# Performance work log

Hardware: AMD Instinct MI355X
Metric: run time of the kernel (lower is better)

The kernel has to match this reference:

```python
import jax, jax.numpy as jnp
import numpy as np

D = 1024        # d_hidden
DE = 512        # d_expert (routed)
E = 8           # n_routed_experts
TOP_K = 2
DS = DE * 2     # shared expert width = d_expert * n_shared_experts


def setup_inputs() -> dict:
    key = jax.random.key(0)
    ks = jax.random.split(key, 8)
    s = 1.0 / np.sqrt(D)
    return {
        "x": jax.random.normal(ks[0], (2, 1024, D), dtype=jnp.float32),
        "W_g": jax.random.normal(ks[1], (D, E), dtype=jnp.float32) * s,
        "Wg_e": jax.random.normal(ks[2], (E, D, DE), dtype=jnp.float32) * s,
        "Wu_e": jax.random.normal(ks[3], (E, D, DE), dtype=jnp.float32) * s,
        "Wd_e": jax.random.normal(ks[4], (E, DE, D), dtype=jnp.float32) * (1.0 / np.sqrt(DE)),
        "Wg_s": jax.random.normal(ks[5], (D, DS), dtype=jnp.float32) * s,
        "Wu_s": jax.random.normal(ks[6], (D, DS), dtype=jnp.float32) * s,
        "Wd_s": jax.random.normal(ks[7], (DS, D), dtype=jnp.float32) * (1.0 / np.sqrt(DS)),
    }


def _moe(x, W_g, Wg_e, Wu_e, Wd_e, Wg_s, Wu_s, Wd_s):
    B, T, Dm = x.shape
    N = B * T
    xf = x.reshape(N, Dm)

    # shared expert (SwiGLU)
    shared = (jax.nn.silu(xf @ Wg_s) * (xf @ Wu_s)) @ Wd_s  # [N, D]

    # gating: softmax then top-k (set membership identical to torch sorted=False)
    probs = jax.nn.softmax(xf @ W_g, axis=-1)               # [N, E]
    topk_vals, topk_ids = jax.lax.top_k(probs, TOP_K)       # [N, K]

    # combine weights c[n, e] = sum of topk_vals where routed to expert e
    # (equivalent to the original gather -> weighted scatter_add combine)
    c = jnp.zeros((N, E), dtype=x.dtype)
    c = c.at[jnp.arange(N)[:, None], topk_ids].add(topk_vals)

    # dense per-expert SwiGLU, weighted-combined (same math as gather/scatter loop)
    gate = jax.nn.silu(jnp.einsum('nd,edh->neh', xf, Wg_e))
    up = jnp.einsum('nd,edh->neh', xf, Wu_e)
    routed = jnp.einsum('neh,ne,ehd->nd', gate * up, c, Wd_e)  # [N, D]

    return (shared + routed).reshape(B, T, Dm)


def reference(x, W_g, Wg_e, Wu_e, Wd_e, Wg_s, Wu_s, Wd_s):
    return _moe(x, W_g, Wg_e, Wu_e, Wd_e, Wg_s, Wu_s, Wd_s)
```

## Files before the change

### kernel.cpp

```cpp
#include <hip/hip_runtime.h>
#include <hip/hip_bf16.h>

#define NTOK 2048
#define DIM  1024
#define DEXP 512
#define NEXP 8
#define DSH  1024
#define KH   5120
#define MAXROWS 5120

typedef __hip_bfloat16 bf16;
typedef __attribute__((ext_vector_type(8))) short bf16x8;
typedef __attribute__((ext_vector_type(4))) float floatx4;

__device__ __forceinline__ void gl_lds16(const bf16* g, bf16* l) {
    __builtin_amdgcn_global_load_lds(
        (const __attribute__((address_space(1))) void*)g,
        (__attribute__((address_space(3))) void*)l, 16, 0, 0);
}

__device__ __forceinline__ float b2f(short s) {
    union { float f; unsigned u; } v;
    v.u = ((unsigned)(unsigned short)s) << 16;
    return v.f;
}

struct B4 { bf16 a, b, c, d; };

__global__ __launch_bounds__(256) void gate_logits(const float* __restrict__ x,
                                                   const float* __restrict__ Wg,
                                                   bf16* __restrict__ Xb,
                                                   int2* __restrict__ te,
                                                   float2* __restrict__ tp) {
    int t = blockIdx.x * 4 + (threadIdx.x >> 6);
    int lane = threadIdx.x & 63;
    const float* xr = x + (long)t * DIM;
    bf16* xo = Xb + (long)t * DIM;
    float acc[NEXP] = {0.f, 0.f, 0.f, 0.f, 0.f, 0.f, 0.f, 0.f};
#pragma unroll
    for (int i = 0; i < 4; i++) {
        int d = lane * 4 + i * 256;
        float4 xv = *(const float4*)(xr + d);
        B4 o{__float2bfloat16(xv.x), __float2bfloat16(xv.y),
             __float2bfloat16(xv.z), __float2bfloat16(xv.w)};
        *(B4*)(xo + d) = o;
#pragma unroll
        for (int j = 0; j < 4; j++) {
            float xs = (j == 0) ? xv.x : (j == 1) ? xv.y : (j == 2) ? xv.z : xv.w;
            float4 w0 = *(const float4*)(Wg + (d + j) * NEXP);
            float4 w1 = *(const float4*)(Wg + (d + j) * NEXP + 4);
            acc[0] += xs * w0.x; acc[1] += xs * w0.y; acc[2] += xs * w0.z; acc[3] += xs * w0.w;
            acc[4] += xs * w1.x; acc[5] += xs * w1.y; acc[6] += xs * w1.z; acc[7] += xs * w1.w;
        }
    }
#pragma unroll
    for (int e = 0; e < NEXP; e++)
#pragma unroll
        for (int off = 32; off; off >>= 1)
            acc[e] += __shfl_xor(acc[e], off);
    if (lane == 0) {
        float m = acc[0];
#pragma unroll
        for (int e = 1; e < NEXP; e++) m = fmaxf(m, acc[e]);
        float p[NEXP], s = 0.f;
#pragma unroll
        for (int e = 0; e < NEXP; e++) { p[e] = expf(acc[e] - m); s += p[e]; }
        float inv = 1.f / s;
#pragma unroll
        for (int e = 0; e < NEXP; e++) p[e] *= inv;
        int i1 = 0;
#pragma unroll
        for (int e = 1; e < NEXP; e++) if (p[e] > p[i1]) i1 = e;
        int i2 = (i1 == 0) ? 1 : 0;
#pragma unroll
        for (int e = 0; e < NEXP; e++) if (e != i1 && p[e] > p[i2]) i2 = e;
        te[t] = make_int2(i1, i2);
        tp[t] = make_float2(p[i1], p[i2]);
    }
}

__global__ __launch_bounds__(512) void assign_kernel(const int2* __restrict__ te,
                                                     const float2* __restrict__ tp,
                                                     int* __restrict__ counts,
                                                     int* __restrict__ offs,
                                                     int* __restrict__ tok_list,
                                                     float* __restrict__ cw,
                                                     int* __restrict__ s1a,
                                                     int* __restrict__ s2a) {
    __shared__ int cnt[NEXP];
    const int e = threadIdx.x >> 6;
    const int lane = threadIdx.x & 63;
    int base = 0;
    for (int t0 = 0; t0 < NTOK; t0 += 64) {
        int t = t0 + lane;
        int2 ee = te[t];
        bool m1 = (ee.x == e), m2 = (ee.y == e);
        bool mt = m1 || m2;
        unsigned long long mask = __ballot(mt);
        int pre = __popcll(mask & ((1ull << lane) - 1ull));
        if (mt) {
            int slot = base + pre;
            tok_list[e * NTOK + slot] = t;
            float2 pp = tp[t];
            cw[e * NTOK + slot] = m1 ? pp.x : pp.y;
            if (m1) s1a[t] = slot; else s2a[t] = slot;
        }
        base += __popcll(mask);
    }
    if (lane == 0) cnt[e] = base;
    __syncthreads();
    if (threadIdx.x == 0) {
        int o = 0;
#pragma unroll
        for (int i = 0; i < NEXP; i++) {
            counts[i] = cnt[i];
            offs[i] = o;
            o += (cnt[i] + 127) & ~127;
        }
    }
}

__global__ __launch_bounds__(256) void pack_weights(
        const float* __restrict__ Wg_s, const float* __restrict__ Wu_s,
        const float* __restrict__ Wg_e, const float* __restrict__ Wu_e,
        const float* __restrict__ Wd_s, const float* __restrict__ Wd_e,
        bf16* __restrict__ Bg, bf16* __restrict__ Bu, bf16* __restrict__ Bd) {
    __shared__ float t[32][36];
    int b = blockIdx.x;
    const float* src; bf16* dst; int C; long dstStride, dstBase; int tilesX;
    if (b < 1024)       { src = Wg_s; dst = Bg; C = 1024; dstStride = 1024; dstBase = 0; tilesX = 32; }
    else if (b < 2048)  { b -= 1024; src = Wu_s; dst = Bu; C = 1024; dstStride = 1024; dstBase = 0; tilesX = 32; }
    else if (b < 6144)  { b -= 2048; int z = b >> 9; b &= 511;
                          src = Wg_e + (long)z * DIM * DEXP; dst = Bg; C = 512;
                          dstStride = 1024; dstBase = (long)(DSH + z * DEXP) * 1024; tilesX = 16; }
    else if (b < 10240) { b -= 6144; int z = b >> 9; b &= 511;
                          src = Wu_e + (long)z * DIM * DEXP; dst = Bu; C = 512;
                          dstStride = 1024; dstBase = (long)(DSH + z * DEXP) * 1024; tilesX = 16; }
    else if (b < 11264) { b -= 10240; src = Wd_s; dst = Bd; C = 1024; dstStride = KH; dstBase = 0; tilesX = 32; }
    else                { b -= 11264; int z = b >> 9; b &= 511;
                          src = Wd_e + (long)z * DEXP * DIM; dst = Bd; C = 1024;
                          dstStride = KH; dstBase = DSH + (long)z * DEXP; tilesX = 32; }
    int tileX = b & (tilesX - 1), tileY = b / tilesX;
    int c0 = tileX * 32, r0 = tileY * 32;

    {
        int row = threadIdx.x >> 3, ch = threadIdx.x & 7;
        float4 v = *(const float4*)(src + (long)(r0 + row) * C + c0 + ch * 4);
        *(float4*)(&t[row][ch * 4]) = v;
    }
    __syncthreads();
    {
        int dc = threadIdx.x & 31, ch = threadIdx.x >> 5;
        int j = ch * 4;
        B4 o{__float2bfloat16(t[j][dc]), __float2bfloat16(t[j + 1][dc]),
             __float2bfloat16(t[j + 2][dc]), __float2bfloat16(t[j + 3][dc])};
        *(B4*)(dst + dstBase + (long)(c0 + dc) * dstStride + r0 + j) = o;
    }
}

__global__ __launch_bounds__(256) void gu_all(const bf16* __restrict__ X,
                                              const bf16* __restrict__ Bg,
                                              const bf16* __restrict__ Bu,
                                              const int* __restrict__ counts,
                                              const int* __restrict__ offs,
                                              const int* __restrict__ tok_list,
                                              const float* __restrict__ cw,
                                              bf16* __restrict__ Hs,
                                              bf16* __restrict__ He) {
    __shared__ __align__(16) bf16 sA[128 * 32];
    __shared__ __align__(16) bf16 sBg[64 * 32];
    __shared__ __align__(16) bf16 sBu[64 * 32];

    const int b = blockIdx.x;
    const bool routed = b < 1024;
    int e = 0, m, c;
    if (routed) {
        e = b >> 7; m = (b >> 3) & 15; c = b & 7;
        if (m * 128 >= counts[e]) return;
    } else {
        int bs = b - 1024; m = bs >> 4; c = bs & 15;
    }
    const int so = routed ? offs[e] : 0;
    const int colB0 = routed ? (DSH + e * DEXP + c * 64) : c * 64;

    const int tid = threadIdx.x;
    const int wave = tid >> 6, lane = tid & 63;
    const int wr = wave >> 1, wc = wave & 1;
    const int q = lane >> 4, l15 = lane & 15;
    const int koff = (q ^ ((l15 >> 1) & 3)) * 8;

    const int r0 = tid >> 2, c4 = tid & 3;
    const int r1 = r0 + 64;
    const int c4s = c4 ^ ((r0 >> 1) & 3);
    long aRow0, aRow1;
    if (routed) {
        const int* tl = tok_list + e * NTOK + m * 128;
        aRow0 = (long)tl[r0] * DIM;
        aRow1 = (long)tl[r1] * DIM;
    } else {
        aRow0 = (long)(m * 128 + r0) * DIM;
        aRow1 = (long)(m * 128 + r1) * DIM;
    }
    const long bRow = (long)(colB0 + r0) * DIM;

    floatx4 accG[4][2], accU[4][2];
    const floatx4 z4 = {0.f, 0.f, 0.f, 0.f};
#pragma unroll
    for (int i = 0; i < 4; i++)
#pragma unroll
        for (int j = 0; j < 2; j++) { accG[i][j] = z4; accU[i][j] = z4; }

    for (int k0 = 0; k0 < DIM; k0 += 32) {
        gl_lds16(X + aRow0 + k0 + c4s * 8, sA + (wave * 64) * 8);
        gl_lds16(X + aRow1 + k0 + c4s * 8, sA + (256 + wave * 64) * 8);
        gl_lds16(Bg + bRow + k0 + c4s * 8, sBg + (wave * 64) * 8);
        gl_lds16(Bu + bRow + k0 + c4s * 8, sBu + (wave * 64) * 8);
        __syncthreads();

        bf16x8 af[4], bg[2], bu[2];
#pragma unroll
        for (int rt = 0; rt < 4; rt++)
            af[rt] = *(const bf16x8*)(sA + (wr * 64 + rt * 16 + l15) * 32 + koff);
#pragma unroll
        for (int ct = 0; ct < 2; ct++) {
            int cb = (wc * 32 + ct * 16 + l15) * 32 + koff;
            bg[ct] = *(const bf16x8*)(sBg + cb);
            bu[ct] = *(const bf16x8*)(sBu + cb);
        }
#pragma unroll
        for (int rt = 0; rt < 4; rt++)
#pragma unroll
            for (int ct = 0; ct < 2; ct++) {
                accG[rt][ct] = __builtin_amdgcn_mfma_f32_16x16x32_bf16(af[rt], bg[ct], accG[rt][ct], 0, 0, 0);
                accU[rt][ct] = __builtin_amdgcn_mfma_f32_16x16x32_bf16(af[rt], bu[ct], accU[rt][ct], 0, 0, 0);
            }
        __syncthreads();
    }

    float wv[4][4];
#pragma unroll
    for (int rt = 0; rt < 4; rt++)
#pragma unroll
        for (int r = 0; r < 4; r++) {
            int srow = wr * 64 + rt * 16 + q * 4 + r;
            wv[rt][r] = routed ? cw[e * NTOK + m * 128 + srow] : 1.0f;
        }
#pragma unroll
    for (int rt = 0; rt < 4; rt++)
#pragma unroll
        for (int ct = 0; ct < 2; ct++)
#pragma unroll
            for (int r = 0; r < 4; r++) {
                int srow = wr * 64 + rt * 16 + q * 4 + r;
                int colLoc = c * 64 + wc * 32 + ct * 16 + l15;
                float g = accG[rt][ct][r];
                float u = accU[rt][ct][r];
                float h = (g / (1.f + __expf(-g))) * u * wv[rt][r];
                if (routed)
                    He[(long)(so + m * 128 + srow) * DEXP + colLoc] = __float2bfloat16(h);
                else
                    Hs[(long)(m * 128 + srow) * DSH + colLoc] = __float2bfloat16(h);
            }
}

__global__ __launch_bounds__(256) void down_all(const bf16* __restrict__ Hs,
                                                const bf16* __restrict__ He,
                                                const bf16* __restrict__ Bd,
                                                const int* __restrict__ counts,
                                                const int* __restrict__ offs,
                                                bf16* __restrict__ Ys,
                                                bf16* __restrict__ Ye) {
    __shared__ __align__(16) bf16 sA[128 * 32];
    __shared__ __align__(16) bf16 sB[64 * 32];

    const int b = blockIdx.x;
    const bool routed = b < 2048;
    int e = 0, m, cc;
    if (routed) {
        e = b >> 8; m = (b >> 4) & 15; cc = b & 15;
        if (m * 128 >= counts[e]) return;
    } else {
        int bs = b - 2048; m = bs >> 4; cc = bs & 15;
    }
    const int so = routed ? offs[e] : 0;
    const bf16* A = routed ? He + (long)so * DEXP : Hs;
    bf16* Y = routed ? Ye + (long)so * DIM : Ys;
    const int astr = routed ? DEXP : DSH;
    const int ksteps = routed ? (DEXP / 32) : (DSH / 32);
    const int kg0 = routed ? (DSH + e * DEXP) : 0;

    const int tid = threadIdx.x;
    const int wave = tid >> 6, lane = tid & 63;
    const int wr = wave >> 1, wc = wave & 1;
    const int q = lane >> 4, l15 = lane & 15;
    const int koff = (q ^ ((l15 >> 1) & 3)) * 8;

    const int r0 = tid >> 2, c4 = tid & 3;
    const int r1 = r0 + 64;
    const int c4s = c4 ^ ((r0 >> 1) & 3);
    const long aRow0 = (long)(m * 128 + r0) * astr;
    const long aRow1 = (long)(m * 128 + r1) * astr;
    const long bRow = (long)(cc * 64 + r0) * KH + kg0;

    floatx4 acc[4][2];
    const floatx4 z4 = {0.f, 0.f, 0.f, 0.f};
#pragma unroll
    for (int i = 0; i < 4; i++)
#pragma unroll
        for (int j = 0; j < 2; j++) acc[i][j] = z4;

    for (int ks = 0; ks < ksteps; ks++) {
        const int k0 = ks * 32;
        gl_lds16(A + aRow0 + k0 + c4s * 8, sA + (wave * 64) * 8);
        gl_lds16(A + aRow1 + k0 + c4s * 8, sA + (256 + wave * 64) * 8);
        gl_lds16(Bd + bRow + k0 + c4s * 8, sB + (wave * 64) * 8);
        __syncthreads();

        bf16x8 af[4], bb[2];
#pragma unroll
        for (int rt = 0; rt < 4; rt++)
            af[rt] = *(const bf16x8*)(sA + (wr * 64 + rt * 16 + l15) * 32 + koff);
#pragma unroll
        for (int ct = 0; ct < 2; ct++)
            bb[ct] = *(const bf16x8*)(sB + (wc * 32 + ct * 16 + l15) * 32 + koff);
#pragma unroll
        for (int rt = 0; rt < 4; rt++)
#pragma unroll
            for (int ct = 0; ct < 2; ct++)
                acc[rt][ct] = __builtin_amdgcn_mfma_f32_16x16x32_bf16(af[rt], bb[ct], acc[rt][ct], 0, 0, 0);
        __syncthreads();
    }

#pragma unroll
    for (int rt = 0; rt < 4; rt++)
#pragma unroll
        for (int ct = 0; ct < 2; ct++)
#pragma unroll
            for (int r = 0; r < 4; r++) {
                int srow = wr * 64 + rt * 16 + q * 4 + r;
                int mc = cc * 64 + wc * 32 + ct * 16 + l15;
                Y[(long)(m * 128 + srow) * DIM + mc] = __float2bfloat16(acc[rt][ct][r]);
            }
}

__global__ __launch_bounds__(256) void combine_kernel(const bf16* __restrict__ Ys,
                                                      const bf16* __restrict__ Ye,
                                                      const int2* __restrict__ te,
                                                      const int* __restrict__ s1a,
                                                      const int* __restrict__ s2a,
                                                      const int* __restrict__ offs,
                                                      float* __restrict__ out) {
    int idx = blockIdx.x * 256 + threadIdx.x;
    int t = idx >> 7;
    int d = (idx & 127) * 8;
    int2 ee = te[t];
    long r1 = (long)(offs[ee.x] + s1a[t]);
    long r2 = (long)(offs[ee.y] + s2a[t]);
    bf16x8 a = *(const bf16x8*)(Ys + (long)t * DIM + d);
    bf16x8 p = *(const bf16x8*)(Ye + r1 * DIM + d);
    bf16x8 r = *(const bf16x8*)(Ye + r2 * DIM + d);
    float* o = out + (long)t * DIM + d;
#pragma unroll
    for (int i = 0; i < 8; i++)
        o[i] = b2f(a[i]) + b2f(p[i]) + b2f(r[i]);
}

extern "C" void kernel_launch(void* const* d_in, const int* in_sizes, int n_in,
                              void* d_out, int out_size, void* d_ws, size_t ws_size,
                              hipStream_t stream) {
    const float* x    = (const float*)d_in[0];
    const float* W_g  = (const float*)d_in[1];
    const float* Wg_e = (const float*)d_in[2];
    const float* Wu_e = (const float*)d_in[3];
    const float* Wd_e = (const float*)d_in[4];
    const float* Wg_s = (const float*)d_in[5];
    const float* Wu_s = (const float*)d_in[6];
    const float* Wd_s = (const float*)d_in[7];
    float* out = (float*)d_out;

    bf16* Xb = (bf16*)d_ws;
    bf16* Bg = Xb + (size_t)NTOK * DIM;
    bf16* Bu = Bg + (size_t)KH * DIM;
    bf16* Bd = Bu + (size_t)KH * DIM;
    bf16* Hs = Bd + (size_t)DIM * KH;
    bf16* He = Hs + (size_t)NTOK * DSH;
    bf16* Ys = He + (size_t)MAXROWS * DEXP;
    bf16* Ye = Ys + (size_t)NTOK * DIM;
    int*  counts   = (int*)(Ye + (size_t)MAXROWS * DIM);
    int*  offs     = counts + NEXP;
    int*  tok_list = offs + NEXP;
    float* cw      = (float*)(tok_list + NEXP * NTOK);
    int*  s1a      = (int*)(cw + NEXP * NTOK);
    int*  s2a      = s1a + NTOK;
    int2* te       = (int2*)(s2a + NTOK);
    float2* tp     = (float2*)(te + NTOK);

    hipMemsetAsync(tok_list, 0,
                   sizeof(int) * NEXP * NTOK + sizeof(float) * NEXP * NTOK, stream);
    gate_logits<<<NTOK / 4, 256, 0, stream>>>(x, W_g, Xb, te, tp);
    assign_kernel<<<1, 512, 0, stream>>>(te, tp, counts, offs, tok_list, cw, s1a, s2a);
    pack_weights<<<15360, 256, 0, stream>>>(Wg_s, Wu_s, Wg_e, Wu_e, Wd_s, Wd_e, Bg, Bu, Bd);
    gu_all<<<1280, 256, 0, stream>>>(Xb, Bg, Bu, counts, offs, tok_list, cw, Hs, He);
    down_all<<<2304, 256, 0, stream>>>(Hs, He, Bd, counts, offs, Ys, Ye);
    combine_kernel<<<NTOK * DIM / 8 / 256, 256, 0, stream>>>(Ys, Ye, te, s1a, s2a, offs, out);
}
```

Baseline: 208.2 us.

## Fuse weight packing with gating, widen transpose tiles, double-buffer GEMM LDS stages

Merges the weight-pack/transposition kernel and the gate-logits kernel into one launch, with blocks split by index. The transpose tile grows from 32x32 to 64x64 with padded LDS and 16-byte bf16 stores. Both GEMM kernels (gate/up and down) now double-buffer their LDS tiles so the next k-step's global-to-LDS load overlaps the current MFMA step, removing one barrier per iteration. This costs twice the LDS per block, which may lower occupancy.

```diff
diff --git a/kernel.cpp b/kernel.cpp
--- a/kernel.cpp
+++ b/kernel.cpp
@@ -8,6 +8,7 @@
 #define DSH  1024
 #define KH   5120
 #define MAXROWS 5120
+#define PACKBLOCKS 3840
 
 typedef __hip_bfloat16 bf16;
 typedef __attribute__((ext_vector_type(8))) short bf16x8;
@@ -27,55 +28,97 @@
 
 struct B4 { bf16 a, b, c, d; };
 
-__global__ __launch_bounds__(256) void gate_logits(const float* __restrict__ x,
-                                                   const float* __restrict__ Wg,
-                                                   bf16* __restrict__ Xb,
-                                                   int2* __restrict__ te,
-                                                   float2* __restrict__ tp) {
-    int t = blockIdx.x * 4 + (threadIdx.x >> 6);
-    int lane = threadIdx.x & 63;
-    const float* xr = x + (long)t * DIM;
-    bf16* xo = Xb + (long)t * DIM;
-    float acc[NEXP] = {0.f, 0.f, 0.f, 0.f, 0.f, 0.f, 0.f, 0.f};
-#pragma unroll
-    for (int i = 0; i < 4; i++) {
-        int d = lane * 4 + i * 256;
-        float4 xv = *(const float4*)(xr + d);
-        B4 o{__float2bfloat16(xv.x), __float2bfloat16(xv.y),
-             __float2bfloat16(xv.z), __float2bfloat16(xv.w)};
-        *(B4*)(xo + d) = o;
-#pragma unroll
-        for (int j = 0; j < 4; j++) {
-            float xs = (j == 0) ? xv.x : (j == 1) ? xv.y : (j == 2) ? xv.z : xv.w;
-            float4 w0 = *(const float4*)(Wg + (d + j) * NEXP);
-            float4 w1 = *(const float4*)(Wg + (d + j) * NEXP + 4);
-            acc[0] += xs * w0.x; acc[1] += xs * w0.y; acc[2] += xs * w0.z; acc[3] += xs * w0.w;
-            acc[4] += xs * w1.x; acc[5] += xs * w1.y; acc[6] += xs * w1.z; acc[7] += xs * w1.w;
-        }
-    }
-#pragma unroll
-    for (int e = 0; e < NEXP; e++)
-#pragma unroll
-        for (int off = 32; off; off >>= 1)
-            acc[e] += __shfl_xor(acc[e], off);
-    if (lane == 0) {
-        float m = acc[0];
-#pragma unroll
-        for (int e = 1; e < NEXP; e++) m = fmaxf(m, acc[e]);
-        float p[NEXP], s = 0.f;
-#pragma unroll
-        for (int e = 0; e < NEXP; e++) { p[e] = expf(acc[e] - m); s += p[e]; }
-        float inv = 1.f / s;
-#pragma unroll
-        for (int e = 0; e < NEXP; e++) p[e] *= inv;
-        int i1 = 0;
-#pragma unroll
-        for (int e = 1; e < NEXP; e++) if (p[e] > p[i1]) i1 = e;
-        int i2 = (i1 == 0) ? 1 : 0;
-#pragma unroll
-        for (int e = 0; e < NEXP; e++) if (e != i1 && p[e] > p[i2]) i2 = e;
-        te[t] = make_int2(i1, i2);
-        tp[t] = make_float2(p[i1], p[i2]);
+__global__ __launch_bounds__(256) void pack_gate(
+        const float* __restrict__ Wg_s, const float* __restrict__ Wu_s,
+        const float* __restrict__ Wg_e, const float* __restrict__ Wu_e,
+        const float* __restrict__ Wd_s, const float* __restrict__ Wd_e,
+        const float* __restrict__ x, const float* __restrict__ Wg,
+        bf16* __restrict__ Bg, bf16* __restrict__ Bu, bf16* __restrict__ Bd,
+        bf16* __restrict__ Xb, int2* __restrict__ te, float2* __restrict__ tp) {
+    int b = blockIdx.x;
+    const int tid = threadIdx.x;
+    if (b < PACKBLOCKS) {
+        __shared__ float t[64][65];
+        const float* src; bf16* dst; int C; long dstStride, dstBase; int tilesX;
+        if (b < 256)        { src = Wg_s; dst = Bg; C = 1024; dstStride = 1024; dstBase = 0; tilesX = 16; }
+        else if (b < 1280)  { int z = (b - 256) >> 7; b = (b - 256) & 127;
+                              src = Wg_e + (long)z * DIM * DEXP; dst = Bg; C = 512;
+                              dstStride = 1024; dstBase = (long)(DSH + z * DEXP) * 1024; tilesX = 8; }
+        else if (b < 1536)  { b -= 1280; src = Wu_s; dst = Bu; C = 1024; dstStride = 1024; dstBase = 0; tilesX = 16; }
+        else if (b < 2560)  { int z = (b - 1536) >> 7; b = (b - 1536) & 127;
+                              src = Wu_e + (long)z * DIM * DEXP; dst = Bu; C = 512;
+                              dstStride = 1024; dstBase = (long)(DSH + z * DEXP) * 1024; tilesX = 8; }
+        else if (b < 2816)  { b -= 2560; src = Wd_s; dst = Bd; C = 1024; dstStride = KH; dstBase = 0; tilesX = 16; }
+        else                { int z = (b - 2816) >> 7; b = (b - 2816) & 127;
+                              src = Wd_e + (long)z * DEXP * DIM; dst = Bd; C = 1024;
+                              dstStride = KH; dstBase = DSH + (long)z * DEXP; tilesX = 16; }
+        const int tileX = b & (tilesX - 1), tileY = b / tilesX;
+        const int c0 = tileX * 64, r0 = tileY * 64;
+
+#pragma unroll
+        for (int i = 0; i < 4; i++) {
+            int row = (tid >> 4) + i * 16;
+            int ch = tid & 15;
+            float4 v = *(const float4*)(src + (long)(r0 + row) * C + c0 + ch * 4);
+            t[row][ch * 4 + 0] = v.x; t[row][ch * 4 + 1] = v.y;
+            t[row][ch * 4 + 2] = v.z; t[row][ch * 4 + 3] = v.w;
+        }
+        __syncthreads();
+#pragma unroll
+        for (int i = 0; i < 2; i++) {
+            int h = (tid >> 3) + i * 32;
+            int kc = tid & 7;
+            union { bf16 s[8]; bf16x8 v; } o;
+#pragma unroll
+            for (int j = 0; j < 8; j++) o.s[j] = __float2bfloat16(t[kc * 8 + j][h]);
+            *(bf16x8*)(dst + dstBase + (long)(c0 + h) * dstStride + r0 + kc * 8) = o.v;
+        }
+    } else {
+        int t = (b - PACKBLOCKS) * 4 + (tid >> 6);
+        int lane = tid & 63;
+        const float* xr = x + (long)t * DIM;
+        bf16* xo = Xb + (long)t * DIM;
+        float acc[NEXP] = {0.f, 0.f, 0.f, 0.f, 0.f, 0.f, 0.f, 0.f};
+#pragma unroll
+        for (int i = 0; i < 4; i++) {
+            int d = lane * 4 + i * 256;
+            float4 xv = *(const float4*)(xr + d);
+            B4 o{__float2bfloat16(xv.x), __float2bfloat16(xv.y),
+                 __float2bfloat16(xv.z), __float2bfloat16(xv.w)};
+            *(B4*)(xo + d) = o;
+#pragma unroll
+            for (int j = 0; j < 4; j++) {
+                float xs = (j == 0) ? xv.x : (j == 1) ? xv.y : (j == 2) ? xv.z : xv.w;
+                float4 w0 = *(const float4*)(Wg + (d + j) * NEXP);
+                float4 w1 = *(const float4*)(Wg + (d + j) * NEXP + 4);
+                acc[0] += xs * w0.x; acc[1] += xs * w0.y; acc[2] += xs * w0.z; acc[3] += xs * w0.w;
+                acc[4] += xs * w1.x; acc[5] += xs * w1.y; acc[6] += xs * w1.z; acc[7] += xs * w1.w;
+            }
+        }
+#pragma unroll
+        for (int e = 0; e < NEXP; e++)
+#pragma unroll
+            for (int off = 32; off; off >>= 1)
+                acc[e] += __shfl_xor(acc[e], off);
+        if (lane == 0) {
+            float m = acc[0];
+#pragma unroll
+            for (int e = 1; e < NEXP; e++) m = fmaxf(m, acc[e]);
+            float p[NEXP], s = 0.f;
+#pragma unroll
+            for (int e = 0; e < NEXP; e++) { p[e] = expf(acc[e] - m); s += p[e]; }
+            float inv = 1.f / s;
+#pragma unroll
+            for (int e = 0; e < NEXP; e++) p[e] *= inv;
+            int i1 = 0;
+#pragma unroll
+            for (int e = 1; e < NEXP; e++) if (p[e] > p[i1]) i1 = e;
+            int i2 = (i1 == 0) ? 1 : 0;
+#pragma unroll
+            for (int e = 0; e < NEXP; e++) if (e != i1 && p[e] > p[i2]) i2 = e;
+            te[t] = make_int2(i1, i2);
+            tp[t] = make_float2(p[i1], p[i2]);
+        }
     }
 }
 
@@ -120,44 +163,6 @@
     }
 }
 
-__global__ __launch_bounds__(256) void pack_weights(
-        const float* __restrict__ Wg_s, const float* __restrict__ Wu_s,
-        const float* __restrict__ Wg_e, const float* __restrict__ Wu_e,
-        const float* __restrict__ Wd_s, const float* __restrict__ Wd_e,
-        bf16* __restrict__ Bg, bf16* __restrict__ Bu, bf16* __restrict__ Bd) {
-    __shared__ float t[32][36];
-    int b = blockIdx.x;
-    const float* src; bf16* dst; int C; long dstStride, dstBase; int tilesX;
-    if (b < 1024)       { src = Wg_s; dst = Bg; C = 1024; dstStride = 1024; dstBase = 0; tilesX = 32; }
-    else if (b < 2048)  { b -= 1024; src = Wu_s; dst = Bu; C = 1024; dstStride = 1024; dstBase = 0; tilesX = 32; }
-    else if (b < 6144)  { b -= 2048; int z = b >> 9; b &= 511;
-                          src = Wg_e + (long)z * DIM * DEXP; dst = Bg; C = 512;
-                          dstStride = 1024; dstBase = (long)(DSH + z * DEXP) * 1024; tilesX = 16; }
-    else if (b < 10240) { b -= 6144; int z = b >> 9; b &= 511;
-                          src = Wu_e + (long)z * DIM * DEXP; dst = Bu; C = 512;
-                          dstStride = 1024; dstBase = (long)(DSH + z * DEXP) * 1024; tilesX = 16; }
-    else if (b < 11264) { b -= 10240; src = Wd_s; dst = Bd; C = 1024; dstStride = KH; dstBase = 0; tilesX = 32; }
-    else                { b -= 11264; int z = b >> 9; b &= 511;
-                          src = Wd_e + (long)z * DEXP * DIM; dst = Bd; C = 1024;
-                          dstStride = KH; dstBase = DSH + (long)z * DEXP; tilesX = 32; }
-    int tileX = b & (tilesX - 1), tileY = b / tilesX;
-    int c0 = tileX * 32, r0 = tileY * 32;
-
-    {
-        int row = threadIdx.x >> 3, ch = threadIdx.x & 7;
-        float4 v = *(const float4*)(src + (long)(r0 + row) * C + c0 + ch * 4);
-        *(float4*)(&t[row][ch * 4]) = v;
-    }
-    __syncthreads();
-    {
-        int dc = threadIdx.x & 31, ch = threadIdx.x >> 5;
-        int j = ch * 4;
-        B4 o{__float2bfloat16(t[j][dc]), __float2bfloat16(t[j + 1][dc]),
-             __float2bfloat16(t[j + 2][dc]), __float2bfloat16(t[j + 3][dc])};
-        *(B4*)(dst + dstBase + (long)(c0 + dc) * dstStride + r0 + j) = o;
-    }
-}
-
 __global__ __launch_bounds__(256) void gu_all(const bf16* __restrict__ X,
                                               const bf16* __restrict__ Bg,
                                               const bf16* __restrict__ Bu,
@@ -167,9 +172,9 @@
                                               const float* __restrict__ cw,
                                               bf16* __restrict__ Hs,
                                               bf16* __restrict__ He) {
-    __shared__ __align__(16) bf16 sA[128 * 32];
-    __shared__ __align__(16) bf16 sBg[64 * 32];
-    __shared__ __align__(16) bf16 sBu[64 * 32];
+    __shared__ __align__(16) bf16 sA[2][128 * 32];
+    __shared__ __align__(16) bf16 sBg[2][64 * 32];
+    __shared__ __align__(16) bf16 sBu[2][64 * 32];
 
     const int b = blockIdx.x;
     const bool routed = b < 1024;
@@ -210,31 +215,40 @@
 #pragma unroll
         for (int j = 0; j < 2; j++) { accG[i][j] = z4; accU[i][j] = z4; }
 
-    for (int k0 = 0; k0 < DIM; k0 += 32) {
-        gl_lds16(X + aRow0 + k0 + c4s * 8, sA + (wave * 64) * 8);
-        gl_lds16(X + aRow1 + k0 + c4s * 8, sA + (256 + wave * 64) * 8);
-        gl_lds16(Bg + bRow + k0 + c4s * 8, sBg + (wave * 64) * 8);
-        gl_lds16(Bu + bRow + k0 + c4s * 8, sBu + (wave * 64) * 8);
-        __syncthreads();
-
-        bf16x8 af[4], bg[2], bu[2];
+    auto stage = [&](int bb, int k0) {
+        gl_lds16(X + aRow0 + k0 + c4s * 8, &sA[bb][wave * 512]);
+        gl_lds16(X + aRow1 + k0 + c4s * 8, &sA[bb][2048 + wave * 512]);
+        gl_lds16(Bg + bRow + k0 + c4s * 8, &sBg[bb][wave * 512]);
+        gl_lds16(Bu + bRow + k0 + c4s * 8, &sBu[bb][wave * 512]);
+    };
+    auto compute = [&](int bb) {
+        bf16x8 af[4], bgv[2], buv[2];
 #pragma unroll
         for (int rt = 0; rt < 4; rt++)
-            af[rt] = *(const bf16x8*)(sA + (wr * 64 + rt * 16 + l15) * 32 + koff);
+            af[rt] = *(const bf16x8*)(&sA[bb][(wr * 64 + rt * 16 + l15) * 32 + koff]);
 #pragma unroll
         for (int ct = 0; ct < 2; ct++) {
             int cb = (wc * 32 + ct * 16 + l15) * 32 + koff;
-            bg[ct] = *(const bf16x8*)(sBg + cb);
-            bu[ct] = *(const bf16x8*)(sBu + cb);
+            bgv[ct] = *(const bf16x8*)(&sBg[bb][cb]);
+            buv[ct] = *(const bf16x8*)(&sBu[bb][cb]);
         }
 #pragma unroll
         for (int rt = 0; rt < 4; rt++)
 #pragma unroll
             for (int ct = 0; ct < 2; ct++) {
-                accG[rt][ct] = __builtin_amdgcn_mfma_f32_16x16x32_bf16(af[rt], bg[ct], accG[rt][ct], 0, 0, 0);
-                accU[rt][ct] = __builtin_amdgcn_mfma_f32_16x16x32_bf16(af[rt], bu[ct], accU[rt][ct], 0, 0, 0);
+                accG[rt][ct] = __builtin_amdgcn_mfma_f32_16x16x32_bf16(af[rt], bgv[ct], accG[rt][ct], 0, 0, 0);
+                accU[rt][ct] = __builtin_amdgcn_mfma_f32_16x16x32_bf16(af[rt], buv[ct], accU[rt][ct], 0, 0, 0);
             }
+    };
+
+    stage(0, 0);
+    __syncthreads();
+    int cur = 0;
+    for (int ks = 0; ks < DIM / 32; ks++) {
+        if (ks < DIM / 32 - 1) stage(cur ^ 1, (ks + 1) * 32);
+        compute(cur);
         __syncthreads();
+        cur ^= 1;
     }
 
     float wv[4][4];
@@ -270,8 +284,8 @@
                                                 const int* __restrict__ offs,
                                                 bf16* __restrict__ Ys,
                                                 bf16* __restrict__ Ye) {
-    __shared__ __align__(16) bf16 sA[128 * 32];
-    __shared__ __align__(16) bf16 sB[64 * 32];
+    __shared__ __align__(16) bf16 sA[2][128 * 32];
+    __shared__ __align__(16) bf16 sB[2][64 * 32];
 
     const int b = blockIdx.x;
     const bool routed = b < 2048;
@@ -309,26 +323,34 @@
 #pragma unroll
         for (int j = 0; j < 2; j++) acc[i][j] = z4;
 
+    auto stage = [&](int bb, int k0) {
+        gl_lds16(A + aRow0 + k0 + c4s * 8, &sA[bb][wave * 512]);
+        gl_lds16(A + aRow1 + k0 + c4s * 8, &sA[bb][2048 + wave * 512]);
+        gl_lds16(Bd + bRow + k0 + c4s * 8, &sB[bb][wave * 512]);
+    };
+    auto compute = [&](int bb) {
+        bf16x8 af[4], bb2[2];
+#pragma unroll
+        for (int rt = 0; rt < 4; rt++)
+            af[rt] = *(const bf16x8*)(&sA[bb][(wr * 64 + rt * 16 + l15) * 32 + koff]);
+#pragma unroll
+        for (int ct = 0; ct < 2; ct++)
+            bb2[ct] = *(const bf16x8*)(&sB[bb][(wc * 32 + ct * 16 + l15) * 32 + koff]);
+#pragma unroll
+        for (int rt = 0; rt < 4; rt++)
+#pragma unroll
+            for (int ct = 0; ct < 2; ct++)
+                acc[rt][ct] = __builtin_amdgcn_mfma_f32_16x16x32_bf16(af[rt], bb2[ct], acc[rt][ct], 0, 0, 0);
+    };
+
+    stage(0, 0);
+    __syncthreads();
+    int cur = 0;
     for (int ks = 0; ks < ksteps; ks++) {
-        const int k0 = ks * 32;
-        gl_lds16(A + aRow0 + k0 + c4s * 8, sA + (wave * 64) * 8);
-        gl_lds16(A + aRow1 + k0 + c4s * 8, sA + (256 + wave * 64) * 8);
-        gl_lds16(Bd + bRow + k0 + c4s * 8, sB + (wave * 64) * 8);
+        if (ks < ksteps - 1) stage(cur ^ 1, (ks + 1) * 32);
+        compute(cur);
         __syncthreads();
-
-        bf16x8 af[4], bb[2];
-#pragma unroll
-        for (int rt = 0; rt < 4; rt++)
-            af[rt] = *(const bf16x8*)(sA + (wr * 64 + rt * 16 + l15) * 32 + koff);
-#pragma unroll
-        for (int ct = 0; ct < 2; ct++)
-            bb[ct] = *(const bf16x8*)(sB + (wc * 32 + ct * 16 + l15) * 32 + koff);
-#pragma unroll
-        for (int rt = 0; rt < 4; rt++)
-#pragma unroll
-            for (int ct = 0; ct < 2; ct++)
-                acc[rt][ct] = __builtin_amdgcn_mfma_f32_16x16x32_bf16(af[rt], bb[ct], acc[rt][ct], 0, 0, 0);
-        __syncthreads();
+        cur ^= 1;
     }
 
 #pragma unroll
@@ -397,9 +419,9 @@
 
     hipMemsetAsync(tok_list, 0,
                    sizeof(int) * NEXP * NTOK + sizeof(float) * NEXP * NTOK, stream);
-    gate_logits<<<NTOK / 4, 256, 0, stream>>>(x, W_g, Xb, te, tp);
+    pack_gate<<<PACKBLOCKS + NTOK / 4, 256, 0, stream>>>(
+        Wg_s, Wu_s, Wg_e, Wu_e, Wd_s, Wd_e, x, W_g, Bg, Bu, Bd, Xb, te, tp);
     assign_kernel<<<1, 512, 0, stream>>>(te, tp, counts, offs, tok_list, cw, s1a, s2a);
-    pack_weights<<<15360, 256, 0, stream>>>(Wg_s, Wu_s, Wg_e, Wu_e, Wd_s, Wd_e, Bg, Bu, Bd);
     gu_all<<<1280, 256, 0, stream>>>(Xb, Bg, Bu, counts, offs, tok_list, cw, Hs, He);
     down_all<<<2304, 256, 0, stream>>>(Hs, He, Bd, counts, offs, Ys, Ye);
     combine_kernel<<<NTOK * DIM / 8 / 256, 256, 0, stream>>>(Ys, Ye, te, s1a, s2a, offs, out);
```

New measurement: 215.8 us. 1.04x slower.
